# Kernel optimization log

Measured on AMD Instinct MI355X. Metric: run time of the kernel, lower is better.

Reference implementation:

```python
import jax, jax.numpy as jnp
import numpy as np

B, T, N_EMBD, HEAD = 8, 2048, 1024, 64
NEG_INF = -1e30  # stand-in for float('-inf'), safe under fp16/bf16 after where


def setup_inputs() -> dict:
    key = jax.random.key(0)
    k0, k1, k2, k3 = jax.random.split(key, 4)
    idx = jax.random.normal(k0, (B, T, N_EMBD), dtype=jnp.float32)
    # nn.Linear weights have shape (out_features, in_features)
    Wk = jax.random.normal(k1, (HEAD, N_EMBD), dtype=jnp.float32) * 0.02
    Wq = jax.random.normal(k2, (HEAD, N_EMBD), dtype=jnp.float32) * 0.02
    Wv = jax.random.normal(k3, (HEAD, N_EMBD), dtype=jnp.float32) * 0.02
    return {"idx": idx, "Wk": Wk, "Wq": Wq, "Wv": Wv}


def reference(idx, Wk, Wq, Wv):
    # idx: [B,T,C]; W*: [H,C] (torch Linear layout, y = x @ W.T)
    Tn = idx.shape[1]
    k = jnp.einsum('btc,hc->bth', idx, Wk)
    q = jnp.einsum('btc,hc->bth', idx, Wq)
    v = jnp.einsum('btc,hc->bth', idx, Wv)
    # NOTE: original has NO 1/sqrt(head_size) scaling
    wei = jnp.einsum('bth,bsh->bts', q, k)  # [B,T,T]
    causal = jnp.tril(jnp.ones((Tn, Tn), dtype=bool))  # keep where tril != 0
    wei = jnp.where(causal[None, :, :], wei, NEG_INF)
    # NOTE: original softmaxes over dim=1 (query axis), not the last axis
    wei = jax.nn.softmax(wei, axis=1)
    out = jnp.einsum('bts,bsh->bth', wei, v)  # [B,T,H]
    return out
```

## Files before the change

kernel.cpp:

```cpp
#include <hip/hip_runtime.h>


typedef __attribute__((ext_vector_type(8))) short bf16x8;
typedef __attribute__((ext_vector_type(4))) float f32x4;
typedef unsigned short u16;

#define MFMA(a, b, c) __builtin_amdgcn_mfma_f32_16x16x32_bf16((a), (b), (c), 0, 0, 0)

__device__ __forceinline__ u16 f2bf(float x) {
    unsigned u = __float_as_uint(x);
    u += 0x7fff + ((u >> 16) & 1);
    return (u16)(u >> 16);
}
__device__ __forceinline__ float bf2f(u16 h) {
    return __uint_as_float(((unsigned)h) << 16);
}

__device__ __forceinline__ void split8(const f32x4 x0, const f32x4 x1,
                                       bf16x8* hv, bf16x8* lv)
{
    const float f[8] = {x0[0], x0[1], x0[2], x0[3], x1[0], x1[1], x1[2], x1[3]};
    union { unsigned u[4]; bf16x8 v; } H, L;
    #pragma unroll
    for (int j = 0; j < 4; ++j) {
        const unsigned u0 = __float_as_uint(f[2 * j]);
        const unsigned u1 = __float_as_uint(f[2 * j + 1]);
        H.u[j] = __builtin_amdgcn_perm(u1, u0, 0x07060302);
        const float l0 = f[2 * j]     - __uint_as_float(u0 & 0xffff0000u);
        const float l1 = f[2 * j + 1] - __uint_as_float(u1 & 0xffff0000u);
        L.u[j] = __builtin_amdgcn_perm(__float_as_uint(l1), __float_as_uint(l0),
                                       0x07060302);
    }
    *hv = H.v;
    *lv = L.v;
}

typedef const __attribute__((address_space(1))) void* gas_p;
typedef __attribute__((address_space(3))) void* las_p;

#define WH_OFF  0u
#define WL_OFF  (WH_OFF + 192u*1024u*2u)
#define FQH_OFF (WL_OFF + 192u*1024u*2u)
#define FQL_OFF (FQH_OFF + 2u*1024u*1024u)
#define FKH_OFF (FQL_OFF + 2u*1024u*1024u)
#define FKL_OFF (FKH_OFF + 2u*1024u*1024u)
#define VF_OFF  (FKL_OFF + 2u*1024u*1024u)
#define DD_OFF  (VF_OFF + 2u*1024u*1024u)
#define PF_OFF  (DD_OFF + 8u*2048u*4u)

__global__ __launch_bounds__(128) void wsplit_kernel(
    const float* __restrict__ Wk, const float* __restrict__ Wq,
    const float* __restrict__ Wv, u16* __restrict__ FWH)
{
    const int n = blockIdx.x;
    const int nblk = n >> 4, lr = n & 15;
    const float* src = (n < 64) ? (Wq + (long)n * 1024)
                     : (n < 128) ? (Wk + (long)(n - 64) * 1024)
                                 : (Wv + (long)(n - 128) * 1024);
    const int f = threadIdx.x;
    const int kc = f >> 2, q = f & 3;
    const float4 f0 = *(const float4*)&src[kc * 32 + q * 8];
    const float4 f1 = *(const float4*)&src[kc * 32 + q * 8 + 4];
    const float vs[8] = {f0.x, f0.y, f0.z, f0.w, f1.x, f1.y, f1.z, f1.w};
    bf16x8 hv;
    #pragma unroll
    for (int j = 0; j < 8; ++j) hv[j] = (short)f2bf(vs[j]);
    const long o = ((long)(nblk * 32 + kc) * 64 + q * 16 + lr) * 8;
    *(bf16x8*)&FWH[o] = hv;
}

__global__ __launch_bounds__(512, 2) void qkv_kernel(
    const float* __restrict__ idx, const u16* __restrict__ FWH,
    u16* __restrict__ FQH, u16* __restrict__ FKH, u16* __restrict__ VF)
{
    __shared__ __align__(16) char smem[3][40960];
    const int tid = threadIdx.x;
    const int w = tid >> 6, lr = tid & 15, quad = (tid >> 4) & 3;
    const int lane = tid & 63;
    const int r0 = blockIdx.x * 64;
    const int b = r0 >> 11, t0 = r0 & 2047;
    const int m0 = (w & 1) * 32;
    const int nbb = (w >> 1) * 3;

    const float* asrc[2];
    int adst[2];
    #pragma unroll
    for (int j = 0; j < 2; ++j) {
        const int s = w * 2 + j;
        const int row = s * 4 + (lane >> 4);
        const int lc = (lane & 15) ^ (row & 7);
        asrc[j] = idx + (long)(r0 + row) * 1024 + lc * 4;
        adst[j] = s * 1024;
    }
    const u16* fsrc[3];
    int fdst[3];
    #pragma unroll
    for (int j = 0; j < 3; ++j) {
        const int seg = w * 3 + j;
        const int nblk = seg >> 1, kcl = seg & 1;
        fsrc[j] = FWH + (long)nblk * 16384 + kcl * 512 + lane * 8;
        fdst[j] = 16384 + seg * 1024;
    }

#define ISSUE(PH)                                                             \
    {                                                                         \
        const int nb_ = (PH) % 3;                                             \
        _Pragma("unroll")                                                     \
        for (int j = 0; j < 2; ++j)                                           \
            __builtin_amdgcn_global_load_lds((gas_p)(asrc[j] + (PH) * 64),    \
                (las_p)(smem[nb_] + adst[j]), 16, 0, 0);                      \
        _Pragma("unroll")                                                     \
        for (int j = 0; j < 3; ++j)                                           \
            __builtin_amdgcn_global_load_lds((gas_p)(fsrc[j] + (long)(PH) * 1024), \
                (las_p)(smem[nb_] + fdst[j]), 16, 0, 0);                      \
    }

#define COMPUTE(PH)                                                           \
    {                                                                         \
        const int nb_ = (PH) % 3;                                             \
        const float* A_ = (const float*)smem[nb_];                            \
        const u16* F_ = (const u16*)(smem[nb_] + 16384);                      \
        _Pragma("unroll")                                                     \
        for (int kc = 0; kc < 2; ++kc) {                                      \
            bf16x8 AH[2], AL[2];                                              \
            _Pragma("unroll")                                                 \
            for (int mi = 0; mi < 2; ++mi) {                                  \
                const int R = m0 + mi * 16 + lr;                              \
                const int c0 = (kc * 8 + quad * 2) ^ (lr & 7);                \
                const f32x4 x0 = *(const f32x4*)&A_[R * 64 + c0 * 4];         \
                const f32x4 x1 = *(const f32x4*)&A_[R * 64 + (c0 ^ 1) * 4];   \
                split8(x0, x1, &AH[mi], &AL[mi]);                             \
            }                                                                 \
            _Pragma("unroll")                                                 \
            for (int nf = 0; nf < 3; ++nf) {                                  \
                const int sb = (((nbb + nf) * 2 + kc)) * 512 + lane * 8;      \
                const bf16x8 bh = *(const bf16x8*)&F_[sb];                    \
                _Pragma("unroll")                                             \
                for (int mi = 0; mi < 2; ++mi) {                              \
                    f32x4 c = acc[mi][nf];                                    \
                    c = MFMA(AH[mi], bh, c);                                  \
                    c = MFMA(AL[mi], bh, c);                                  \
                    acc[mi][nf] = c;                                          \
                }                                                             \
            }                                                                 \
        }                                                                     \
    }

#define WAITV(N)                                                              \
    asm volatile("s_waitcnt vmcnt(" #N ")" ::: "memory");                     \
    __builtin_amdgcn_sched_barrier(0);                                        \
    __builtin_amdgcn_s_barrier();

    f32x4 acc[2][3] = {};

    ISSUE(0); ISSUE(1);
    WAITV(5)

    for (int ph = 0; ph < 14; ++ph) {
        ISSUE(ph + 2);
        __builtin_amdgcn_sched_barrier(0);
        COMPUTE(ph);
        WAITV(5)
    }
    COMPUTE(14);
    WAITV(0)
    COMPUTE(15);

#undef WAITV
#undef COMPUTE
#undef ISSUE

    #pragma unroll
    for (int mi = 0; mi < 2; ++mi) {
        const int tb = t0 + m0 + mi * 16 + quad * 4;
        const int tblk = (t0 + m0 + mi * 16) >> 4;
        #pragma unroll
        for (int nf = 0; nf < 3; ++nf) {
            const int n = (nbb + nf) * 16 + lr;
            const f32x4 a = acc[mi][nf];
            if (n < 128) {
                u16* Hd = (n < 64) ? FQH : FKH;
                const int h = n & 63;
                const int kc = h >> 5;
                const int lsub = 16 * ((h & 31) >> 3);
                const long base = ((long)(b * 128 + tblk) * 2 + kc) * 512 + (h & 7);
                #pragma unroll
                for (int r = 0; r < 4; ++r) {
                    const long o = base + (long)(quad * 4 + r + lsub) * 8;
                    Hd[o] = f2bf(a[r]);
                }
            } else {
                const int h = n - 128;
                const int hblk = h >> 4;
                #pragma unroll
                for (int r = 0; r < 4; ++r) {
                    const int t = tb + r;
                    const long o = ((long)(b * 4 + hblk) * 64 + (t >> 5)) * 512
                                 + (long)(16 * ((t & 31) >> 3) + (h & 15)) * 8 + (t & 7);
                    VF[o] = f2bf(a[r]);
                }
            }
        }
    }
}

__global__ __launch_bounds__(256, 4) void stats_kernel(
    const u16* __restrict__ FQH, const u16* __restrict__ FKH,
    u16* __restrict__ PF, float* __restrict__ D)
{
    __shared__ float red[4][64];
    const int tid = threadIdx.x;
    const int w = tid >> 6, lr = tid & 15, quad = (tid >> 4) & 3;
    const int lane = tid & 63;
    const int b = blockIdx.y;
    int x = blockIdx.x, i = 0;
    for (;;) { const int nc = (39 - i) >> 3; if (x < nc) break; x -= nc; ++i; }
    const int s0 = i * 64;
    const int jt0 = i + 8 * x, jt1 = min(jt0 + 8, 32);

    uint2* __restrict__ PQ = (uint2*)PF;

    bf16x8 KH[4][2];
    #pragma unroll
    for (int sf = 0; sf < 4; ++sf) {
        const long kb = ((long)(b * 128 + i * 4 + sf) * 2) * 512 + lane * 8;
        KH[sf][0] = *(const bf16x8*)&FKH[kb];
        KH[sf][1] = *(const bf16x8*)&FKH[kb + 512];
    }

    float dsum[4][4] = {};
    for (int jt = jt0; jt < jt1; ++jt) {
        const long qb = ((long)(b * 128 + jt * 4 + w) * 2) * 512 + lane * 8;
        const bf16x8 qh0 = *(const bf16x8*)&FQH[qb];
        const bf16x8 qh1 = *(const bf16x8*)&FQH[qb + 512];
        const bool diag = (jt == i);
        const int t_sub = w * 16 + lr;
        const long tb_base = ((long)(b * 128 + jt * 4 + w)) * 512;
        #pragma unroll
        for (int sf = 0; sf < 4; ++sf) {
            f32x4 cc = {};
            cc = MFMA(KH[sf][0], qh0, cc);
            cc = MFMA(KH[sf][1], qh1, cc);

            u16 hq[4];
            #pragma unroll
            for (int r = 0; r < 4; ++r) {
                float ev = __expf(cc[r]);
                if (diag && (t_sub < sf * 16 + quad * 4 + r)) ev = 0.f;
                dsum[sf][r] += ev;
                hq[r] = f2bf(ev);
            }
            uint2 pk;
            pk.x = (unsigned)hq[0] | ((unsigned)hq[1] << 16);
            pk.y = (unsigned)hq[2] | ((unsigned)hq[3] << 16);
            PQ[(tb_base + i * 16 + sf * 4 + quad) * 16 + lr] = pk;
        }
    }

    #pragma unroll
    for (int sf = 0; sf < 4; ++sf)
        #pragma unroll
        for (int r = 0; r < 4; ++r) {
            float v = dsum[sf][r];
            v += __shfl_xor(v, 1);
            v += __shfl_xor(v, 2);
            v += __shfl_xor(v, 4);
            v += __shfl_xor(v, 8);
            dsum[sf][r] = v;
        }
    if (lr == 0) {
        #pragma unroll
        for (int sf = 0; sf < 4; ++sf)
            #pragma unroll
            for (int r = 0; r < 4; ++r)
                red[w][sf * 16 + quad * 4 + r] = dsum[sf][r];
    }
    __syncthreads();
    if (tid < 64)
        atomicAdd(&D[b * 2048 + s0 + tid],
                  red[0][tid] + red[1][tid] + red[2][tid] + red[3][tid]);
}

__global__ __launch_bounds__(256, 4) void out_kernel(
    const u16* __restrict__ PF, const u16* __restrict__ VF,
    const float* __restrict__ D, float* __restrict__ out)
{
    const int tid = threadIdx.x;
    const int w = tid >> 6, lr = tid & 15, quad = (tid >> 4) & 3;
    const int lane = tid & 63;
    const int b = blockIdx.y;
    int x = blockIdx.x, i = 0;
    for (;;) { const int nc = (i + 8) >> 3; if (x < nc) break; x -= nc; ++i; }
    const int t0 = i * 64;
    const int js0 = 8 * x, js1 = min(8 * x + 8, i + 1);
    const int tblk = i * 4 + w;

    const uint2* __restrict__ PQ = (const uint2*)PF;
    const int g = lane >> 4, tr = lane & 15;
    const long tb_base = ((long)(b * 128 + tblk)) * 512;

    f32x4 oacc[4] = {};
    for (int js = js0; js < js1; ++js) {
        bf16x8 pa[2];
        #pragma unroll
        for (int kcp = 0; kcp < 2; ++kcp) {
            const long u = (tb_base + js * 16 + kcp * 8 + g * 2) * 16 + tr;
            const uint2 a0 = PQ[u];
            const uint2 a1 = PQ[u + 16];
            union { unsigned uu[4]; bf16x8 v; } P_;
            P_.uu[0] = a0.x; P_.uu[1] = a0.y; P_.uu[2] = a1.x; P_.uu[3] = a1.y;
            const int sb = js * 64 + kcp * 32 + g * 8;
            const float4 d0 = *(const float4*)&D[b * 2048 + sb];
            const float4 d1 = *(const float4*)&D[b * 2048 + sb + 4];
            const float dv[8] = {d0.x, d0.y, d0.z, d0.w, d1.x, d1.y, d1.z, d1.w};
            bf16x8 sc;
            #pragma unroll
            for (int j = 0; j < 8; ++j)
                sc[j] = (short)f2bf(bf2f((u16)P_.v[j]) *
                                    __builtin_amdgcn_rcpf(dv[j]));
            pa[kcp] = sc;
        }
        #pragma unroll
        for (int nf = 0; nf < 4; ++nf) {
            const long vb = ((long)(b * 4 + nf) * 64 + 2 * js) * 512 + lane * 8;
            const bf16x8 v0 = *(const bf16x8*)&VF[vb];
            const bf16x8 v1 = *(const bf16x8*)&VF[vb + 512];
            oacc[nf] = MFMA(pa[0], v0, oacc[nf]);
            oacc[nf] = MFMA(pa[1], v1, oacc[nf]);
        }
    }

    const bool single = (i < 8);
    #pragma unroll
    for (int nf = 0; nf < 4; ++nf) {
        const int h = nf * 16 + lr;
        #pragma unroll
        for (int r = 0; r < 4; ++r) {
            const int t = t0 + w * 16 + quad * 4 + r;
            const long o = (long)(b * 2048 + t) * 64 + h;
            if (single) out[o] = oacc[nf][r];
            else        atomicAdd(&out[o], oacc[nf][r]);
        }
    }
}

extern "C" void kernel_launch(void* const* d_in, const int* in_sizes, int n_in,
                              void* d_out, int out_size, void* d_ws, size_t ws_size,
                              hipStream_t stream)
{
    const float* idx = (const float*)d_in[0];
    const float* Wk  = (const float*)d_in[1];
    const float* Wq  = (const float*)d_in[2];
    const float* Wv  = (const float*)d_in[3];
    char* ws = (char*)d_ws;
    float* out = (float*)d_out;

    u16* FWH = (u16*)(ws + WH_OFF);
    u16* FQH = (u16*)(ws + FQH_OFF);
    u16* FKH = (u16*)(ws + FKH_OFF);
    u16* VF  = (u16*)(ws + VF_OFF);
    float* Dp = (float*)(ws + DD_OFF);
    u16* PF  = (u16*)(ws + PF_OFF);

    hipMemsetAsync(out, 0, (size_t)8 * 2048 * 64 * sizeof(float), stream);
    hipMemsetAsync(Dp, 0, (size_t)8 * 2048 * sizeof(float), stream);

    wsplit_kernel<<<192, 128, 0, stream>>>(Wk, Wq, Wv, FWH);
    qkv_kernel<<<256, 512, 0, stream>>>(idx, FWH, FQH, FKH, VF);
    stats_kernel<<<dim3(80, 8), 256, 0, stream>>>(FQH, FKH, PF, Dp);
    out_kernel<<<dim3(80, 8), 256, 0, stream>>>(PF, VF, Dp, out);
}
```

Measured before the change: 142.8 us.

## Halve QKV row tile to 32 and K-step to 32 for more blocks per CU

Each QKV projection block now covers 32 rows instead of 64, and each pipeline stage loads a 32-wide K chunk instead of 64. LDS per stage drops from 40 KB to 16 KB, so the launch bound rises to 4 blocks per CU and the grid doubles to 512 blocks, which gives better occupancy and fills all CUs. Loading is split by wave: waves 0-1 fetch the fp32 activations and the remaining waves fetch the packed weights. In exchange, each weight fragment feeds half as many MFMAs, so weights are re-read from global memory twice as often, and the loop needs twice as many barriers.

```diff
diff --git a/kernel.cpp b/kernel.cpp
--- a/kernel.cpp
+++ b/kernel.cpp
@@ -69,80 +69,67 @@
     *(bf16x8*)&FWH[o] = hv;
 }
 
-__global__ __launch_bounds__(512, 2) void qkv_kernel(
+__global__ __launch_bounds__(512, 4) void qkv_kernel(
     const float* __restrict__ idx, const u16* __restrict__ FWH,
     u16* __restrict__ FQH, u16* __restrict__ FKH, u16* __restrict__ VF)
 {
-    __shared__ __align__(16) char smem[3][40960];
+    __shared__ __align__(16) char smem[3][16384];
     const int tid = threadIdx.x;
     const int w = tid >> 6, lr = tid & 15, quad = (tid >> 4) & 3;
     const int lane = tid & 63;
-    const int r0 = blockIdx.x * 64;
+    const int r0 = blockIdx.x * 32;
     const int b = r0 >> 11, t0 = r0 & 2047;
-    const int m0 = (w & 1) * 32;
+    const int m0 = (w & 1) * 16;
     const int nbb = (w >> 1) * 3;
 
-    const float* asrc[2];
-    int adst[2];
+    const void* gsrc[2];
+    int gdst[2];
     #pragma unroll
     for (int j = 0; j < 2; ++j) {
-        const int s = w * 2 + j;
-        const int row = s * 4 + (lane >> 4);
-        const int lc = (lane & 15) ^ (row & 7);
-        asrc[j] = idx + (long)(r0 + row) * 1024 + lc * 4;
-        adst[j] = s * 1024;
-    }
-    const u16* fsrc[3];
-    int fdst[3];
-    #pragma unroll
-    for (int j = 0; j < 3; ++j) {
-        const int seg = w * 3 + j;
-        const int nblk = seg >> 1, kcl = seg & 1;
-        fsrc[j] = FWH + (long)nblk * 16384 + kcl * 512 + lane * 8;
-        fdst[j] = 16384 + seg * 1024;
-    }
+        if (w < 2) {
+            const int s = w * 2 + j;
+            const int row = s * 8 + (lane >> 3);
+            const int lc = (lane & 7) ^ (row & 7);
+            gsrc[j] = (const void*)(idx + (long)(r0 + row) * 1024 + lc * 4);
+            gdst[j] = s * 1024;
+        } else {
+            const int fi = (w - 2) * 2 + j;
+            gsrc[j] = (const void*)(FWH + (long)fi * 16384 + lane * 8);
+            gdst[j] = 4096 + fi * 1024;
+        }
+    }
+    const int gadv = (w < 2) ? 128 : 1024;
 
 #define ISSUE(PH)                                                             \
     {                                                                         \
         const int nb_ = (PH) % 3;                                             \
         _Pragma("unroll")                                                     \
         for (int j = 0; j < 2; ++j)                                           \
-            __builtin_amdgcn_global_load_lds((gas_p)(asrc[j] + (PH) * 64),    \
-                (las_p)(smem[nb_] + adst[j]), 16, 0, 0);                      \
-        _Pragma("unroll")                                                     \
-        for (int j = 0; j < 3; ++j)                                           \
-            __builtin_amdgcn_global_load_lds((gas_p)(fsrc[j] + (long)(PH) * 1024), \
-                (las_p)(smem[nb_] + fdst[j]), 16, 0, 0);                      \
+            __builtin_amdgcn_global_load_lds(                                 \
+                (gas_p)((const char*)gsrc[j] + (long)(PH) * gadv),            \
+                (las_p)(smem[nb_] + gdst[j]), 16, 0, 0);                      \
     }
 
 #define COMPUTE(PH)                                                           \
     {                                                                         \
         const int nb_ = (PH) % 3;                                             \
         const float* A_ = (const float*)smem[nb_];                            \
-        const u16* F_ = (const u16*)(smem[nb_] + 16384);                      \
+        const u16* F_ = (const u16*)(smem[nb_] + 4096);                       \
+        bf16x8 AH, AL;                                                        \
+        {                                                                     \
+            const int R = m0 + lr;                                            \
+            const int pc0 = (quad * 2) ^ (lr & 7);                            \
+            const f32x4 x0 = *(const f32x4*)&A_[R * 32 + pc0 * 4];            \
+            const f32x4 x1 = *(const f32x4*)&A_[R * 32 + (pc0 ^ 1) * 4];      \
+            split8(x0, x1, &AH, &AL);                                         \
+        }                                                                     \
         _Pragma("unroll")                                                     \
-        for (int kc = 0; kc < 2; ++kc) {                                      \
-            bf16x8 AH[2], AL[2];                                              \
-            _Pragma("unroll")                                                 \
-            for (int mi = 0; mi < 2; ++mi) {                                  \
-                const int R = m0 + mi * 16 + lr;                              \
-                const int c0 = (kc * 8 + quad * 2) ^ (lr & 7);                \
-                const f32x4 x0 = *(const f32x4*)&A_[R * 64 + c0 * 4];         \
-                const f32x4 x1 = *(const f32x4*)&A_[R * 64 + (c0 ^ 1) * 4];   \
-                split8(x0, x1, &AH[mi], &AL[mi]);                             \
-            }                                                                 \
-            _Pragma("unroll")                                                 \
-            for (int nf = 0; nf < 3; ++nf) {                                  \
-                const int sb = (((nbb + nf) * 2 + kc)) * 512 + lane * 8;      \
-                const bf16x8 bh = *(const bf16x8*)&F_[sb];                    \
-                _Pragma("unroll")                                             \
-                for (int mi = 0; mi < 2; ++mi) {                              \
-                    f32x4 c = acc[mi][nf];                                    \
-                    c = MFMA(AH[mi], bh, c);                                  \
-                    c = MFMA(AL[mi], bh, c);                                  \
-                    acc[mi][nf] = c;                                          \
-                }                                                             \
-            }                                                                 \
+        for (int nf = 0; nf < 3; ++nf) {                                      \
+            const bf16x8 bh = *(const bf16x8*)&F_[(nbb + nf) * 512 + lane * 8]; \
+            f32x4 c = acc[nf];                                                \
+            c = MFMA(AH, bh, c);                                              \
+            c = MFMA(AL, bh, c);                                              \
+            acc[nf] = c;                                                      \
         }                                                                     \
     }
 
@@ -151,33 +138,32 @@
     __builtin_amdgcn_sched_barrier(0);                                        \
     __builtin_amdgcn_s_barrier();
 
-    f32x4 acc[2][3] = {};
+    f32x4 acc[3] = {};
 
     ISSUE(0); ISSUE(1);
-    WAITV(5)
-
-    for (int ph = 0; ph < 14; ++ph) {
+    WAITV(2)
+
+    for (int ph = 0; ph < 30; ++ph) {
         ISSUE(ph + 2);
         __builtin_amdgcn_sched_barrier(0);
         COMPUTE(ph);
-        WAITV(5)
-    }
-    COMPUTE(14);
+        WAITV(2)
+    }
+    COMPUTE(30);
     WAITV(0)
-    COMPUTE(15);
+    COMPUTE(31);
 
 #undef WAITV
 #undef COMPUTE
 #undef ISSUE
 
-    #pragma unroll
-    for (int mi = 0; mi < 2; ++mi) {
-        const int tb = t0 + m0 + mi * 16 + quad * 4;
-        const int tblk = (t0 + m0 + mi * 16) >> 4;
+    {
+        const int tb = t0 + m0 + quad * 4;
+        const int tblk = (t0 + m0) >> 4;
         #pragma unroll
         for (int nf = 0; nf < 3; ++nf) {
             const int n = (nbb + nf) * 16 + lr;
-            const f32x4 a = acc[mi][nf];
+            const f32x4 a = acc[nf];
             if (n < 128) {
                 u16* Hd = (n < 64) ? FQH : FKH;
                 const int h = n & 63;
@@ -366,7 +352,7 @@
     hipMemsetAsync(Dp, 0, (size_t)8 * 2048 * sizeof(float), stream);
 
     wsplit_kernel<<<192, 128, 0, stream>>>(Wk, Wq, Wv, FWH);
-    qkv_kernel<<<256, 512, 0, stream>>>(idx, FWH, FQH, FKH, VF);
+    qkv_kernel<<<512, 512, 0, stream>>>(idx, FWH, FQH, FKH, VF);
     stats_kernel<<<dim3(80, 8), 256, 0, stream>>>(FQH, FKH, PF, Dp);
     out_kernel<<<dim3(80, 8), 256, 0, stream>>>(PF, VF, Dp, out);
 }
```

New measurement: 149.8 us. 1.05x slower.

## Recompute QK^T exponentials in out kernel instead of storing P matrix

Applied to the files above, without the earlier changes.

The stats kernel no longer writes the bf16 exp(QK^T) matrix to global memory and only accumulates the column sums. The out kernel recomputes the scores with MFMA, applies the exp, mask and 1/D normalization, and stages the result through a swizzled LDS tile to reach the A-operand layout for the PV MFMA. This removes a large global write and read of the causal P matrix, about 64 MB of traffic, at the cost of doing the QK^T matmul and exp twice. It also adds two block barriers per iteration.

```diff
diff --git a/kernel.cpp b/kernel.cpp
--- a/kernel.cpp
+++ b/kernel.cpp
@@ -39,14 +39,10 @@
 typedef __attribute__((address_space(3))) void* las_p;
 
 #define WH_OFF  0u
-#define WL_OFF  (WH_OFF + 192u*1024u*2u)
-#define FQH_OFF (WL_OFF + 192u*1024u*2u)
-#define FQL_OFF (FQH_OFF + 2u*1024u*1024u)
-#define FKH_OFF (FQL_OFF + 2u*1024u*1024u)
-#define FKL_OFF (FKH_OFF + 2u*1024u*1024u)
-#define VF_OFF  (FKL_OFF + 2u*1024u*1024u)
+#define FQH_OFF (WH_OFF + 2u*192u*1024u*2u)
+#define FKH_OFF (FQH_OFF + 2u*1024u*1024u)
+#define VF_OFF  (FKH_OFF + 2u*1024u*1024u)
 #define DD_OFF  (VF_OFF + 2u*1024u*1024u)
-#define PF_OFF  (DD_OFF + 8u*2048u*4u)
 
 __global__ __launch_bounds__(128) void wsplit_kernel(
     const float* __restrict__ Wk, const float* __restrict__ Wq,
@@ -206,7 +202,7 @@
 
 __global__ __launch_bounds__(256, 4) void stats_kernel(
     const u16* __restrict__ FQH, const u16* __restrict__ FKH,
-    u16* __restrict__ PF, float* __restrict__ D)
+    float* __restrict__ D)
 {
     __shared__ float red[4][64];
     const int tid = threadIdx.x;
@@ -218,8 +214,6 @@
     const int s0 = i * 64;
     const int jt0 = i + 8 * x, jt1 = min(jt0 + 8, 32);
 
-    uint2* __restrict__ PQ = (uint2*)PF;
-
     bf16x8 KH[4][2];
     #pragma unroll
     for (int sf = 0; sf < 4; ++sf) {
@@ -235,25 +229,17 @@
         const bf16x8 qh1 = *(const bf16x8*)&FQH[qb + 512];
         const bool diag = (jt == i);
         const int t_sub = w * 16 + lr;
-        const long tb_base = ((long)(b * 128 + jt * 4 + w)) * 512;
         #pragma unroll
         for (int sf = 0; sf < 4; ++sf) {
             f32x4 cc = {};
             cc = MFMA(KH[sf][0], qh0, cc);
             cc = MFMA(KH[sf][1], qh1, cc);
-
-            u16 hq[4];
             #pragma unroll
             for (int r = 0; r < 4; ++r) {
                 float ev = __expf(cc[r]);
                 if (diag && (t_sub < sf * 16 + quad * 4 + r)) ev = 0.f;
                 dsum[sf][r] += ev;
-                hq[r] = f2bf(ev);
             }
-            uint2 pk;
-            pk.x = (unsigned)hq[0] | ((unsigned)hq[1] << 16);
-            pk.y = (unsigned)hq[2] | ((unsigned)hq[3] << 16);
-            PQ[(tb_base + i * 16 + sf * 4 + quad) * 16 + lr] = pk;
         }
     }
 
@@ -282,9 +268,11 @@
 }
 
 __global__ __launch_bounds__(256, 4) void out_kernel(
-    const u16* __restrict__ PF, const u16* __restrict__ VF,
-    const float* __restrict__ D, float* __restrict__ out)
-{
+    const u16* __restrict__ FQH, const u16* __restrict__ FKH,
+    const u16* __restrict__ VF, const float* __restrict__ D,
+    float* __restrict__ out)
+{
+    __shared__ __align__(16) u16 p_l[64 * 64];
     const int tid = threadIdx.x;
     const int w = tid >> 6, lr = tid & 15, quad = (tid >> 4) & 3;
     const int lane = tid & 63;
@@ -293,32 +281,49 @@
     for (;;) { const int nc = (i + 8) >> 3; if (x < nc) break; x -= nc; ++i; }
     const int t0 = i * 64;
     const int js0 = 8 * x, js1 = min(8 * x + 8, i + 1);
-    const int tblk = i * 4 + w;
-
-    const uint2* __restrict__ PQ = (const uint2*)PF;
-    const int g = lane >> 4, tr = lane & 15;
-    const long tb_base = ((long)(b * 128 + tblk)) * 512;
+
+    const long qb = ((long)(b * 128 + i * 4 + w) * 2) * 512 + lane * 8;
+    const bf16x8 qh0 = *(const bf16x8*)&FQH[qb];
+    const bf16x8 qh1 = *(const bf16x8*)&FQH[qb + 512];
+    const int t_sub = w * 16 + lr;
 
     f32x4 oacc[4] = {};
     for (int js = js0; js < js1; ++js) {
+        const bool diag = (js == i);
+        #pragma unroll
+        for (int sf = 0; sf < 4; ++sf) {
+            const long kb = ((long)(b * 128 + js * 4 + sf) * 2) * 512 + lane * 8;
+            const bf16x8 kh0 = *(const bf16x8*)&FKH[kb];
+            const bf16x8 kh1 = *(const bf16x8*)&FKH[kb + 512];
+            f32x4 cc = {};
+            cc = MFMA(kh0, qh0, cc);
+            cc = MFMA(kh1, qh1, cc);
+
+            const f32x4 dv = *(const f32x4*)&D[b * 2048 + js * 64 + sf * 16 + quad * 4];
+            u16 hq[4];
+            #pragma unroll
+            for (int r = 0; r < 4; ++r) {
+                float ev = __expf(cc[r]);
+                if (diag && (t_sub < sf * 16 + quad * 4 + r)) ev = 0.f;
+                hq[r] = f2bf(ev * __builtin_amdgcn_rcpf(dv[r]));
+            }
+            const int s_sub = sf * 16 + quad * 4;
+            const int ch = (s_sub >> 3) ^ (t_sub & 7);
+            const int aoff = t_sub * 64 + ch * 8 + (s_sub & 7);
+            uint2 pk;
+            pk.x = (unsigned)hq[0] | ((unsigned)hq[1] << 16);
+            pk.y = (unsigned)hq[2] | ((unsigned)hq[3] << 16);
+            *(uint2*)&p_l[aoff] = pk;
+        }
+        __syncthreads();
+
         bf16x8 pa[2];
         #pragma unroll
         for (int kcp = 0; kcp < 2; ++kcp) {
-            const long u = (tb_base + js * 16 + kcp * 8 + g * 2) * 16 + tr;
-            const uint2 a0 = PQ[u];
-            const uint2 a1 = PQ[u + 16];
-            union { unsigned uu[4]; bf16x8 v; } P_;
-            P_.uu[0] = a0.x; P_.uu[1] = a0.y; P_.uu[2] = a1.x; P_.uu[3] = a1.y;
-            const int sb = js * 64 + kcp * 32 + g * 8;
-            const float4 d0 = *(const float4*)&D[b * 2048 + sb];
-            const float4 d1 = *(const float4*)&D[b * 2048 + sb + 4];
-            const float dv[8] = {d0.x, d0.y, d0.z, d0.w, d1.x, d1.y, d1.z, d1.w};
-            bf16x8 sc;
-            #pragma unroll
-            for (int j = 0; j < 8; ++j)
-                sc[j] = (short)f2bf(bf2f((u16)P_.v[j]) *
-                                    __builtin_amdgcn_rcpf(dv[j]));
-            pa[kcp] = sc;
+            const int row = w * 16 + (lane & 15);
+            const int sc = kcp * 32 + (lane >> 4) * 8;
+            const int ch = (sc >> 3) ^ (row & 7);
+            pa[kcp] = *(const bf16x8*)&p_l[row * 64 + ch * 8];
         }
         #pragma unroll
         for (int nf = 0; nf < 4; ++nf) {
@@ -328,6 +333,7 @@
             oacc[nf] = MFMA(pa[0], v0, oacc[nf]);
             oacc[nf] = MFMA(pa[1], v1, oacc[nf]);
         }
+        __syncthreads();
     }
 
     const bool single = (i < 8);
@@ -360,13 +366,12 @@
     u16* FKH = (u16*)(ws + FKH_OFF);
     u16* VF  = (u16*)(ws + VF_OFF);
     float* Dp = (float*)(ws + DD_OFF);
-    u16* PF  = (u16*)(ws + PF_OFF);
 
     hipMemsetAsync(out, 0, (size_t)8 * 2048 * 64 * sizeof(float), stream);
     hipMemsetAsync(Dp, 0, (size_t)8 * 2048 * sizeof(float), stream);
 
     wsplit_kernel<<<192, 128, 0, stream>>>(Wk, Wq, Wv, FWH);
     qkv_kernel<<<256, 512, 0, stream>>>(idx, FWH, FQH, FKH, VF);
-    stats_kernel<<<dim3(80, 8), 256, 0, stream>>>(FQH, FKH, PF, Dp);
-    out_kernel<<<dim3(80, 8), 256, 0, stream>>>(PF, VF, Dp, out);
-}
+    stats_kernel<<<dim3(80, 8), 256, 0, stream>>>(FQH, FKH, Dp);
+    out_kernel<<<dim3(80, 8), 256, 0, stream>>>(FQH, FKH, VF, Dp, out);
+}
```

New measurement: 145.7 us. No clear change (+2.0%).
